# Optimization experiments

Hardware: AMD Instinct MI355X
Metric: run time of the kernel (lower is better)

The kernel has to match this reference:

```python
import jax, jax.numpy as jnp
import numpy as np

K_ORDER = 3
GRID_N = 10
GRID_LO, GRID_HI = -2.0, 2.0
LAYERS = [(49, 256), (256, 256), (256, 10)]
NCOEF = GRID_N + K_ORDER  # 13


def mish(x):
    return x * jnp.tanh(jax.nn.softplus(x))


def bspline_basis(x):
    # x: (B, in) -> basis (B, in, GRID_N + K_ORDER)
    h = (GRID_HI - GRID_LO) / GRID_N
    knots = GRID_LO + h * jnp.arange(-K_ORDER, GRID_N + K_ORDER + 1, dtype=x.dtype)  # (G+2k+1,)
    xx = x[..., None]
    B = ((xx >= knots[:-1]) & (xx < knots[1:])).astype(x.dtype)  # degree-0, (B,in,G+2k)
    for d in range(1, K_ORDER + 1):
        left = (xx - knots[: -(d + 1)]) / (knots[d:-1] - knots[: -(d + 1)]) * B[..., :-1]
        right = (knots[d + 1:] - xx) / (knots[d + 1:] - knots[1:-d]) * B[..., 1:]
        B = left + right
    return B  # (B, in, G+k)


def kan_layer(x, coef, scale_base, scale_sp, bias):
    # x: (B,in); coef: (in,out,G+k); scales: (in,out); bias: (out,)
    basis = bspline_basis(x)                                   # (B,in,G+k)
    spline = jnp.einsum('big,iog->bo', basis, coef * scale_sp[..., None])
    base = jnp.einsum('bi,io->bo', mish(x), scale_base)
    return base + spline + bias


def setup_inputs() -> dict:
    key = jax.random.key(0)
    ks = jax.random.split(key, 1 + 4 * len(LAYERS))
    inp = {'x': jax.random.normal(ks[0], (8192, 1, 28, 28), dtype=jnp.float32)}
    i = 1
    for li, (fin, fout) in enumerate(LAYERS, start=1):
        inp[f'coef{li}'] = 0.1 * jax.random.normal(ks[i], (fin, fout, NCOEF), dtype=jnp.float32); i += 1
        inp[f'sb{li}'] = 1.0 + 0.1 * jax.random.normal(ks[i], (fin, fout), dtype=jnp.float32); i += 1
        inp[f'sp{li}'] = 1.0 + 0.1 * jax.random.normal(ks[i], (fin, fout), dtype=jnp.float32); i += 1
        inp[f'b{li}'] = jnp.zeros((fout,), dtype=jnp.float32); i += 1
    return inp


def reference(x, coef1, sb1, sp1, b1, coef2, sb2, sp2, b2, coef3, sb3, sp3, b3):
    B = x.shape[0]
    # avg_pool2d(x, 4): 28x28 -> 7x7
    h = x.reshape(B, 1, 7, 4, 7, 4).mean(axis=(3, 5))
    h = h.reshape(B, 49)
    h = kan_layer(h, coef1, sb1, sp1, b1)
    h = kan_layer(h, coef2, sb2, sp2, b2)
    h = kan_layer(h, coef3, sb3, sp3, b3)
    return jax.nn.log_softmax(h, axis=1)
```

## Files before the change

### kernel.cpp

```cpp
#include <hip/hip_runtime.h>
#include <hip/hip_bf16.h>

typedef __bf16 bf16x8_t __attribute__((ext_vector_type(8)));
typedef float f32x4_t __attribute__((ext_vector_type(4)));
using bf16 = __hip_bfloat16;

#define ASG __attribute__((address_space(1)))
#define ASL __attribute__((address_space(3)))

__device__ __forceinline__ void gld_lds16(const void* g, void* l) {
  __builtin_amdgcn_global_load_lds((ASG void*)const_cast<void*>(g),
                                   (ASL void*)l, 16, 0, 0);
}

__device__ __forceinline__ unsigned short f2bf_bits(float v) {
  __hip_bfloat16 h = __float2bfloat16(v);
  return *reinterpret_cast<unsigned short*>(&h);
}

__device__ __forceinline__ float mish_f(float x) {
  float z = __expf(x);
  float n = z * (z + 2.0f);
  float m = x * n / (n + 2.0f);
  return (x > 10.0f) ? x : m;
}

__device__ __forceinline__ void kan_feats28(bf16* dst, float x) {
  unsigned int* d32 = (unsigned int*)dst;
#pragma unroll
  for (int d = 0; d < 7; ++d) d32[d] = 0u;
  float t = (x + 3.2f) * 2.5f;
  if (t >= 0.0f && t < 16.0f) {
    float tf = floorf(t);
    int c = (int)tf;
    float u = t - tf;
    float um = 1.0f - u;
    float u2 = u * u, u3 = u2 * u;
    const float s6 = 1.0f / 6.0f;
    float w0 = um * um * um * s6;
    float w1 = (3.0f * u3 - 6.0f * u2 + 4.0f) * s6;
    float w2 = (-3.0f * u3 + 3.0f * u2 + 3.0f * u + 1.0f) * s6;
    float w3 = u3 * s6;
    int j0 = c - 3;
    if (j0 >= 0)               dst[j0]     = __float2bfloat16(w0);
    if (j0 >= -1 && j0 <= 11)  dst[j0 + 1] = __float2bfloat16(w1);
    if (j0 >= -2 && j0 <= 10)  dst[j0 + 2] = __float2bfloat16(w2);
    if (j0 <= 9)               dst[j0 + 3] = __float2bfloat16(w3);
  }
  dst[13] = __float2bfloat16(mish_f(x));
}

__global__ __launch_bounds__(256) void prep_all(
    const float* __restrict__ c1, const float* __restrict__ sb1, const float* __restrict__ sp1,
    const float* __restrict__ c2, const float* __restrict__ sb2, const float* __restrict__ sp2,
    const float* __restrict__ c3, const float* __restrict__ sb3, const float* __restrict__ sp3,
    bf16* __restrict__ W1t, bf16* __restrict__ W2f, bf16* __restrict__ W3f) {
  const int b = blockIdx.x, o = threadIdx.x;
  float vals[14];
  if (b < 49) {
    const int i = b;
    const size_t io = (size_t)i * 256 + o;
    const float spv = sp1[io];
#pragma unroll
    for (int r = 0; r < 13; ++r) vals[r] = c1[io * 13 + r] * spv;
    vals[13] = sb1[io];
    unsigned int* dst = (unsigned int*)(W1t + (size_t)o * 704 + i * 14);
#pragma unroll
    for (int d = 0; d < 7; ++d)
      dst[d] = (unsigned int)f2bf_bits(vals[2 * d]) |
               ((unsigned int)f2bf_bits(vals[2 * d + 1]) << 16);
  } else if (b == 49) {
    unsigned int* dst = (unsigned int*)(W1t + (size_t)o * 704 + 686);
#pragma unroll
    for (int d = 0; d < 9; ++d) dst[d] = 0u;
  } else if (b < 306) {
    const int i = b - 50;
    const size_t io = (size_t)i * 256 + o;
    const float spv = sp2[io];
#pragma unroll
    for (int r = 0; r < 13; ++r) vals[r] = c2[io * 13 + r] * spv;
    vals[13] = sb2[io];
    const int ntg = o >> 4, lr = o & 15;
#pragma unroll
    for (int d = 0; d < 7; ++d) {
      const int k2 = i * 14 + 2 * d;
      const int kc = k2 / 224, rem = k2 % 224;
      const int ks = rem / 32, r2 = rem % 32, quad = r2 / 8, el = r2 % 8;
      const size_t off = ((size_t)((kc * 7 + ks) * 16 + ntg)) * 512 + lr * 32 + quad * 8 + el;
      *(unsigned int*)(W2f + off) = (unsigned int)f2bf_bits(vals[2 * d]) |
                                    ((unsigned int)f2bf_bits(vals[2 * d + 1]) << 16);
    }
  } else {
    const int i = b - 306;
    if (o < 10) {
      const size_t io = (size_t)i * 10 + o;
      const float spv = sp3[io];
#pragma unroll
      for (int r = 0; r < 13; ++r) vals[r] = c3[io * 13 + r] * spv;
      vals[13] = sb3[io];
#pragma unroll
      for (int d = 0; d < 7; ++d) {
        const int k2 = i * 14 + 2 * d;
        const int s = k2 >> 5, r2 = k2 & 31;
        const size_t off = (size_t)s * 512 + o * 32 + (r2 >> 3) * 8 + (r2 & 7);
        *(unsigned int*)(W3f + off) = (unsigned int)f2bf_bits(vals[2 * d]) |
                                      ((unsigned int)f2bf_bits(vals[2 * d + 1]) << 16);
      }
    } else if (o < 16) {
#pragma unroll
      for (int d = 0; d < 7; ++d) {
        const int k2 = i * 14 + 2 * d;
        const int s = k2 >> 5, r2 = k2 & 31;
        *(unsigned int*)(W3f + (size_t)s * 512 + o * 32 + (r2 >> 3) * 8 + (r2 & 7)) = 0u;
      }
    }
  }
}

__global__ __launch_bounds__(256) void pool_basis1(const float* __restrict__ x,
                                                   bf16* __restrict__ A1) {
  __shared__ __align__(16) float xs[3136];
  __shared__ __align__(16) bf16 arow[4 * 704];
  const int b4 = blockIdx.x * 4, t = threadIdx.x;
  const float4* xsrc = (const float4*)(x + (size_t)b4 * 784);
  float4* xd = (float4*)xs;
#pragma unroll
  for (int l = t; l < 784; l += 256) xd[l] = xsrc[l];
  __syncthreads();
  if (t < 196) {
    const int img = t / 49, p = t - img * 49;
    const int oh = p / 7, ow = p - oh * 7;
    const float* xi = xs + img * 784;
    float s = 0.f;
#pragma unroll
    for (int r = 0; r < 4; ++r)
#pragma unroll
      for (int c = 0; c < 4; ++c) s += xi[(oh * 4 + r) * 28 + ow * 4 + c];
    kan_feats28(&arow[img * 704 + p * 14], s * (1.0f / 16.0f));
  } else if (t < 232) {
    const int q = t - 196;
    const int img = q / 9, d = q - img * 9;
    ((unsigned int*)(arow + img * 704 + 686))[d] = 0u;
  }
  __syncthreads();
  uint4* dst = (uint4*)(A1 + (size_t)b4 * 704);
  const uint4* src = (const uint4*)arow;
#pragma unroll
  for (int l = t; l < 352; l += 256) dst[l] = src[l];
}

__global__ __launch_bounds__(256) void gemm1s(
    const bf16* __restrict__ A, const bf16* __restrict__ Wt,
    const float* __restrict__ bias, float* __restrict__ H) {
  constexpr int K = 704;
  __shared__ __align__(16) bf16 As[64 * 64];
  __shared__ __align__(16) bf16 Bs[64 * 64];
  const int t = threadIdx.x;
  const int wv = t >> 6, lane = t & 63, quad = lane >> 4, lr = lane & 15;
  const int n0 = blockIdx.x * 64;
  const int m0 = blockIdx.y * 64;
  const int srow0 = lane >> 3;
  const int cg = (lane & 7) ^ srow0;
  const bf16* gA0 = A + (size_t)(m0 + 8 * wv + srow0) * K + cg * 8;
  const bf16* gA1 = A + (size_t)(m0 + 32 + 8 * wv + srow0) * K + cg * 8;
  const bf16* gB0 = Wt + (size_t)(n0 + 8 * wv + srow0) * K + cg * 8;
  const bf16* gB1 = Wt + (size_t)(n0 + 32 + 8 * wv + srow0) * K + cg * 8;
  char* const lA = (char*)As + wv * 1024;
  char* const lB = (char*)Bs + wv * 1024;
  const int wm = (wv & 1) * 32, wn = (wv >> 1) * 32;
  const int swz = lr & 7;
  f32x4_t acc00 = {0.f, 0.f, 0.f, 0.f}, acc01 = acc00, acc10 = acc00, acc11 = acc00;
  for (int k0 = 0; k0 < K; k0 += 64) {
    gld_lds16(gA0 + k0, lA);
    gld_lds16(gA1 + k0, lA + 4096);
    gld_lds16(gB0 + k0, lB);
    gld_lds16(gB1 + k0, lB + 4096);
    __syncthreads();
#pragma unroll
    for (int s = 0; s < 2; ++s) {
      const int co = ((s * 4 + quad) ^ swz) * 16;
      bf16x8_t a0 = *(const bf16x8_t*)((char*)As + (wm + lr) * 128 + co);
      bf16x8_t a1 = *(const bf16x8_t*)((char*)As + (wm + 16 + lr) * 128 + co);
      bf16x8_t b0 = *(const bf16x8_t*)((char*)Bs + (wn + lr) * 128 + co);
      bf16x8_t b1 = *(const bf16x8_t*)((char*)Bs + (wn + 16 + lr) * 128 + co);
      acc00 = __builtin_amdgcn_mfma_f32_16x16x32_bf16(a0, b0, acc00, 0, 0, 0);
      acc01 = __builtin_amdgcn_mfma_f32_16x16x32_bf16(a0, b1, acc01, 0, 0, 0);
      acc10 = __builtin_amdgcn_mfma_f32_16x16x32_bf16(a1, b0, acc10, 0, 0, 0);
      acc11 = __builtin_amdgcn_mfma_f32_16x16x32_bf16(a1, b1, acc11, 0, 0, 0);
    }
    __syncthreads();
  }
  const int cb = n0 + wn + lr;
  const float bn0 = bias[cb], bn1 = bias[cb + 16];
#pragma unroll
  for (int r = 0; r < 4; ++r) {
    const size_t row = (size_t)(m0 + wm + quad * 4 + r);
    H[row * 256 + cb] = acc00[r] + bn0;
    H[row * 256 + cb + 16] = acc01[r] + bn1;
    H[(row + 16) * 256 + cb] = acc10[r] + bn0;
    H[(row + 16) * 256 + cb + 16] = acc11[r] + bn1;
  }
}

__global__ __launch_bounds__(512, 4) void kan_gemm2(
    const float* __restrict__ Hin, const bf16* __restrict__ W2f,
    float* __restrict__ Hp) {
  __shared__ __align__(16) bf16 As[2][64 * 232];
  const int t = threadIdx.x;
  const int w = t >> 6, lane = t & 63, quad = lane >> 4, lr = lane & 15;
  const int m0 = blockIdx.x * 64;
  const int z = blockIdx.y;
  const int ej = t & 15, er0 = (t >> 4) & 31;
  const int foff = lr * 32 + quad * 8;
  f32x4_t acc[4][2];
#pragma unroll
  for (int m = 0; m < 4; ++m) {
    acc[m][0] = (f32x4_t){0.f, 0.f, 0.f, 0.f};
    acc[m][1] = (f32x4_t){0.f, 0.f, 0.f, 0.f};
  }
  const float* hp = Hin + (size_t)(m0 + er0) * 256 + z * 64 + ej;
  kan_feats28(As[0] + er0 * 232 + ej * 14, hp[0]);
  kan_feats28(As[0] + (er0 + 32) * 232 + ej * 14, hp[32 * 256]);
  const bf16* wbase = W2f + ((size_t)(z * 28 * 16 + w * 2)) * 512 + foff;
  bf16x8_t p0[4], p1[4];
#pragma unroll
  for (int s = 0; s < 4; ++s) {
    p0[s] = *(const bf16x8_t*)(wbase + (size_t)s * 8192);
    p1[s] = *(const bf16x8_t*)(wbase + (size_t)s * 8192 + 512);
  }
#pragma unroll
  for (int kcl = 0; kcl < 4; ++kcl) {
    __syncthreads();
    const bf16* cur = As[kcl & 1];
    bf16* nxt = As[(kcl & 1) ^ 1];
#pragma unroll
    for (int ks = 0; ks < 7; ++ks) {
      const int step = kcl * 7 + ks;
      const int slot = step & 3;
      bf16x8_t b0 = p0[slot], b1 = p1[slot];
      if (step + 4 < 28) {
        p0[slot] = *(const bf16x8_t*)(wbase + (size_t)(step + 4) * 8192);
        p1[slot] = *(const bf16x8_t*)(wbase + (size_t)(step + 4) * 8192 + 512);
      }
#pragma unroll
      for (int m = 0; m < 4; ++m) {
        bf16x8_t a = *(const bf16x8_t*)(cur + (m * 16 + lr) * 232 + ks * 32 + quad * 8);
        acc[m][0] = __builtin_amdgcn_mfma_f32_16x16x32_bf16(a, b0, acc[m][0], 0, 0, 0);
        acc[m][1] = __builtin_amdgcn_mfma_f32_16x16x32_bf16(a, b1, acc[m][1], 0, 0, 0);
      }
    }
    if (kcl < 3) {
      kan_feats28(nxt + er0 * 232 + ej * 14, hp[(kcl + 1) * 16]);
      kan_feats28(nxt + (er0 + 32) * 232 + ej * 14, hp[32 * 256 + (kcl + 1) * 16]);
    }
  }
  float* Hpz = Hp + (size_t)z * (8192 * 256);
  const int c0 = w * 32 + lr;
#pragma unroll
  for (int m = 0; m < 4; ++m)
#pragma unroll
    for (int r = 0; r < 4; ++r) {
      const size_t row = (size_t)(m0 + m * 16 + quad * 4 + r);
      Hpz[row * 256 + c0] = acc[m][0][r];
      Hpz[row * 256 + c0 + 16] = acc[m][1][r];
    }
}

__global__ __launch_bounds__(256) void kan_gemm3(
    const float* __restrict__ Hp, const float* __restrict__ b2,
    const bf16* __restrict__ W3f, float* __restrict__ part) {
  __shared__ __align__(16) bf16 As[64 * 232];
  const int t = threadIdx.x;
  const int wv = t >> 6, lane = t & 63, quad = lane >> 4, lr = lane & 15;
  const int m0 = blockIdx.x * 64;
  const int z = blockIdx.y;
  const int ej = t & 15, er0 = t >> 4;
  const int foff = lr * 32 + quad * 8;
  f32x4_t acc = {0.f, 0.f, 0.f, 0.f};
#pragma unroll
  for (int kcl = 0; kcl < 2; ++kcl) {
    const int kc = z * 2 + kcl;
    const float bc = b2[kc * 16 + ej];
    const float* hp = Hp + (size_t)(m0 + er0) * 256 + kc * 16 + ej;
    if (kcl) __syncthreads();
#pragma unroll
    for (int e = 0; e < 4; ++e) {
      const size_t idx = (size_t)e * 16 * 256;
      float h = hp[idx] + hp[idx + 2097152] + hp[idx + 4194304] + hp[idx + 6291456] + bc;
      kan_feats28(As + (er0 + 16 * e) * 232 + ej * 14, h);
    }
    __syncthreads();
#pragma unroll
    for (int ks = 0; ks < 7; ++ks) {
      bf16x8_t b = *(const bf16x8_t*)(W3f + (size_t)(kc * 7 + ks) * 512 + foff);
      bf16x8_t a = *(const bf16x8_t*)(As + (wv * 16 + lr) * 232 + ks * 32 + quad * 8);
      acc = __builtin_amdgcn_mfma_f32_16x16x32_bf16(a, b, acc, 0, 0, 0);
    }
  }
#pragma unroll
  for (int r = 0; r < 4; ++r)
    part[(size_t)z * 131072 + (size_t)lr * 8192 + (m0 + wv * 16 + quad * 4 + r)] = acc[r];
}

__global__ __launch_bounds__(256) void lsm(const float* __restrict__ part,
                                           const float* __restrict__ b3,
                                           float* __restrict__ out) {
  const int row = blockIdx.x * 256 + threadIdx.x;
  float v[10];
#pragma unroll
  for (int o = 0; o < 10; ++o) {
    float s = b3[o];
#pragma unroll
    for (int kc = 0; kc < 8; ++kc) s += part[(size_t)kc * 131072 + (size_t)o * 8192 + row];
    v[o] = s;
  }
  float m = v[0];
#pragma unroll
  for (int o = 1; o < 10; ++o) m = fmaxf(m, v[o]);
  float se = 0.f;
#pragma unroll
  for (int o = 0; o < 10; ++o) se += expf(v[o] - m);
  const float l = m + logf(se);
#pragma unroll
  for (int o = 0; o < 10; ++o) out[(size_t)row * 10 + o] = v[o] - l;
}

extern "C" void kernel_launch(void* const* d_in, const int* in_sizes, int n_in,
                              void* d_out, int out_size, void* d_ws, size_t ws_size,
                              hipStream_t stream) {
  const float* x = (const float*)d_in[0];
  const float* coef1 = (const float*)d_in[1];
  const float* sb1 = (const float*)d_in[2];
  const float* sp1 = (const float*)d_in[3];
  const float* b1 = (const float*)d_in[4];
  const float* coef2 = (const float*)d_in[5];
  const float* sb2 = (const float*)d_in[6];
  const float* sp2 = (const float*)d_in[7];
  const float* b2 = (const float*)d_in[8];
  const float* coef3 = (const float*)d_in[9];
  const float* sb3 = (const float*)d_in[10];
  const float* sp3 = (const float*)d_in[11];
  const float* b3 = (const float*)d_in[12];
  float* out = (float*)d_out;

  char* ws = (char*)d_ws;
  size_t off = 0;
  bf16* A1 = (bf16*)(ws + off);    off += 11534336;
  bf16* W1t = (bf16*)(ws + off);   off += 360448;
  bf16* W2f = (bf16*)(ws + off);   off += 1835008;
  bf16* W3f = (bf16*)(ws + off);   off += 114688;
  float* H1 = (float*)(ws + off);  off += 8388608;
  float* Hp = (float*)(ws + off);  off += 33554432;
  float* part = (float*)(ws + off); off += 4194304;

  prep_all<<<562, 256, 0, stream>>>(coef1, sb1, sp1, coef2, sb2, sp2,
                                    coef3, sb3, sp3, W1t, W2f, W3f);
  pool_basis1<<<2048, 256, 0, stream>>>(x, A1);
  gemm1s<<<dim3(4, 128), 256, 0, stream>>>(A1, W1t, b1, H1);
  kan_gemm2<<<dim3(128, 4), 512, 0, stream>>>(H1, W2f, Hp);
  kan_gemm3<<<dim3(128, 8), 256, 0, stream>>>(Hp, b2, W3f, part);
  lsm<<<32, 256, 0, stream>>>(part, b3, out);
}
```

Measured before the change: 146.4 us.

## Fuse pooling, three KAN layers and log-softmax into one persistent kernel

Replaces the five-kernel chain (pool+basis, gemm1, gemm2, gemm3, log-softmax) with a single kernel in which each block processes 32 rows end to end. Intermediate activations stay in LDS instead of going through global workspace, and W1 is repacked into the same fragment layout as W2 so it can be streamed from registers. This removes several large global round trips and the launch gaps between kernels. The cost is a grid of only 256 blocks, each using about 120 KB of LDS and doing all the weight reads itself, so occupancy and weight reuse across rows drop.

```diff
diff --git a/kernel.cpp b/kernel.cpp
--- a/kernel.cpp
+++ b/kernel.cpp
@@ -4,14 +4,6 @@
 typedef __bf16 bf16x8_t __attribute__((ext_vector_type(8)));
 typedef float f32x4_t __attribute__((ext_vector_type(4)));
 using bf16 = __hip_bfloat16;
-
-#define ASG __attribute__((address_space(1)))
-#define ASL __attribute__((address_space(3)))
-
-__device__ __forceinline__ void gld_lds16(const void* g, void* l) {
-  __builtin_amdgcn_global_load_lds((ASG void*)const_cast<void*>(g),
-                                   (ASL void*)l, 16, 0, 0);
-}
 
 __device__ __forceinline__ unsigned short f2bf_bits(float v) {
   __hip_bfloat16 h = __float2bfloat16(v);
@@ -54,9 +46,10 @@
     const float* __restrict__ c1, const float* __restrict__ sb1, const float* __restrict__ sp1,
     const float* __restrict__ c2, const float* __restrict__ sb2, const float* __restrict__ sp2,
     const float* __restrict__ c3, const float* __restrict__ sb3, const float* __restrict__ sp3,
-    bf16* __restrict__ W1t, bf16* __restrict__ W2f, bf16* __restrict__ W3f) {
+    bf16* __restrict__ W1f, bf16* __restrict__ W2f, bf16* __restrict__ W3f) {
   const int b = blockIdx.x, o = threadIdx.x;
   float vals[14];
+  const int ntg = o >> 4, lrr = o & 15;
   if (b < 49) {
     const int i = b;
     const size_t io = (size_t)i * 256 + o;
@@ -64,15 +57,21 @@
 #pragma unroll
     for (int r = 0; r < 13; ++r) vals[r] = c1[io * 13 + r] * spv;
     vals[13] = sb1[io];
-    unsigned int* dst = (unsigned int*)(W1t + (size_t)o * 704 + i * 14);
-#pragma unroll
-    for (int d = 0; d < 7; ++d)
-      dst[d] = (unsigned int)f2bf_bits(vals[2 * d]) |
-               ((unsigned int)f2bf_bits(vals[2 * d + 1]) << 16);
+#pragma unroll
+    for (int d = 0; d < 7; ++d) {
+      const int k2 = i * 14 + 2 * d;
+      const int s = k2 >> 5, r2 = k2 & 31;
+      const size_t off = ((size_t)(s * 16 + ntg)) * 512 + lrr * 32 + (r2 >> 3) * 8 + (r2 & 7);
+      *(unsigned int*)(W1f + off) = (unsigned int)f2bf_bits(vals[2 * d]) |
+                                    ((unsigned int)f2bf_bits(vals[2 * d + 1]) << 16);
+    }
   } else if (b == 49) {
-    unsigned int* dst = (unsigned int*)(W1t + (size_t)o * 704 + 686);
-#pragma unroll
-    for (int d = 0; d < 9; ++d) dst[d] = 0u;
+#pragma unroll
+    for (int d = 0; d < 9; ++d) {
+      const int k2 = 686 + 2 * d;
+      const int r2 = k2 & 31;
+      *(unsigned int*)(W1f + ((size_t)(21 * 16 + ntg)) * 512 + lrr * 32 + (r2 >> 3) * 8 + (r2 & 7)) = 0u;
+    }
   } else if (b < 306) {
     const int i = b - 50;
     const size_t io = (size_t)i * 256 + o;
@@ -80,13 +79,11 @@
 #pragma unroll
     for (int r = 0; r < 13; ++r) vals[r] = c2[io * 13 + r] * spv;
     vals[13] = sb2[io];
-    const int ntg = o >> 4, lr = o & 15;
 #pragma unroll
     for (int d = 0; d < 7; ++d) {
       const int k2 = i * 14 + 2 * d;
-      const int kc = k2 / 224, rem = k2 % 224;
-      const int ks = rem / 32, r2 = rem % 32, quad = r2 / 8, el = r2 % 8;
-      const size_t off = ((size_t)((kc * 7 + ks) * 16 + ntg)) * 512 + lr * 32 + quad * 8 + el;
+      const int s = k2 >> 5, r2 = k2 & 31;
+      const size_t off = ((size_t)(s * 16 + ntg)) * 512 + lrr * 32 + (r2 >> 3) * 8 + (r2 & 7);
       *(unsigned int*)(W2f + off) = (unsigned int)f2bf_bits(vals[2 * d]) |
                                     ((unsigned int)f2bf_bits(vals[2 * d + 1]) << 16);
     }
@@ -117,212 +114,215 @@
   }
 }
 
-__global__ __launch_bounds__(256) void pool_basis1(const float* __restrict__ x,
-                                                   bf16* __restrict__ A1) {
-  __shared__ __align__(16) float xs[3136];
-  __shared__ __align__(16) bf16 arow[4 * 704];
-  const int b4 = blockIdx.x * 4, t = threadIdx.x;
-  const float4* xsrc = (const float4*)(x + (size_t)b4 * 784);
-  float4* xd = (float4*)xs;
-#pragma unroll
-  for (int l = t; l < 784; l += 256) xd[l] = xsrc[l];
-  __syncthreads();
-  if (t < 196) {
-    const int img = t / 49, p = t - img * 49;
-    const int oh = p / 7, ow = p - oh * 7;
-    const float* xi = xs + img * 784;
-    float s = 0.f;
-#pragma unroll
-    for (int r = 0; r < 4; ++r)
-#pragma unroll
-      for (int c = 0; c < 4; ++c) s += xi[(oh * 4 + r) * 28 + ow * 4 + c];
-    kan_feats28(&arow[img * 704 + p * 14], s * (1.0f / 16.0f));
-  } else if (t < 232) {
-    const int q = t - 196;
-    const int img = q / 9, d = q - img * 9;
-    ((unsigned int*)(arow + img * 704 + 686))[d] = 0u;
-  }
-  __syncthreads();
-  uint4* dst = (uint4*)(A1 + (size_t)b4 * 704);
-  const uint4* src = (const uint4*)arow;
-#pragma unroll
-  for (int l = t; l < 352; l += 256) dst[l] = src[l];
-}
-
-__global__ __launch_bounds__(256) void gemm1s(
-    const bf16* __restrict__ A, const bf16* __restrict__ Wt,
-    const float* __restrict__ bias, float* __restrict__ H) {
-  constexpr int K = 704;
-  __shared__ __align__(16) bf16 As[64 * 64];
-  __shared__ __align__(16) bf16 Bs[64 * 64];
-  const int t = threadIdx.x;
-  const int wv = t >> 6, lane = t & 63, quad = lane >> 4, lr = lane & 15;
-  const int n0 = blockIdx.x * 64;
-  const int m0 = blockIdx.y * 64;
-  const int srow0 = lane >> 3;
-  const int cg = (lane & 7) ^ srow0;
-  const bf16* gA0 = A + (size_t)(m0 + 8 * wv + srow0) * K + cg * 8;
-  const bf16* gA1 = A + (size_t)(m0 + 32 + 8 * wv + srow0) * K + cg * 8;
-  const bf16* gB0 = Wt + (size_t)(n0 + 8 * wv + srow0) * K + cg * 8;
-  const bf16* gB1 = Wt + (size_t)(n0 + 32 + 8 * wv + srow0) * K + cg * 8;
-  char* const lA = (char*)As + wv * 1024;
-  char* const lB = (char*)Bs + wv * 1024;
-  const int wm = (wv & 1) * 32, wn = (wv >> 1) * 32;
-  const int swz = lr & 7;
-  f32x4_t acc00 = {0.f, 0.f, 0.f, 0.f}, acc01 = acc00, acc10 = acc00, acc11 = acc00;
-  for (int k0 = 0; k0 < K; k0 += 64) {
-    gld_lds16(gA0 + k0, lA);
-    gld_lds16(gA1 + k0, lA + 4096);
-    gld_lds16(gB0 + k0, lB);
-    gld_lds16(gB1 + k0, lB + 4096);
-    __syncthreads();
-#pragma unroll
-    for (int s = 0; s < 2; ++s) {
-      const int co = ((s * 4 + quad) ^ swz) * 16;
-      bf16x8_t a0 = *(const bf16x8_t*)((char*)As + (wm + lr) * 128 + co);
-      bf16x8_t a1 = *(const bf16x8_t*)((char*)As + (wm + 16 + lr) * 128 + co);
-      bf16x8_t b0 = *(const bf16x8_t*)((char*)Bs + (wn + lr) * 128 + co);
-      bf16x8_t b1 = *(const bf16x8_t*)((char*)Bs + (wn + 16 + lr) * 128 + co);
-      acc00 = __builtin_amdgcn_mfma_f32_16x16x32_bf16(a0, b0, acc00, 0, 0, 0);
-      acc01 = __builtin_amdgcn_mfma_f32_16x16x32_bf16(a0, b1, acc01, 0, 0, 0);
-      acc10 = __builtin_amdgcn_mfma_f32_16x16x32_bf16(a1, b0, acc10, 0, 0, 0);
-      acc11 = __builtin_amdgcn_mfma_f32_16x16x32_bf16(a1, b1, acc11, 0, 0, 0);
-    }
-    __syncthreads();
-  }
-  const int cb = n0 + wn + lr;
-  const float bn0 = bias[cb], bn1 = bias[cb + 16];
-#pragma unroll
-  for (int r = 0; r < 4; ++r) {
-    const size_t row = (size_t)(m0 + wm + quad * 4 + r);
-    H[row * 256 + cb] = acc00[r] + bn0;
-    H[row * 256 + cb + 16] = acc01[r] + bn1;
-    H[(row + 16) * 256 + cb] = acc10[r] + bn0;
-    H[(row + 16) * 256 + cb + 16] = acc11[r] + bn1;
-  }
-}
-
-__global__ __launch_bounds__(512, 4) void kan_gemm2(
-    const float* __restrict__ Hin, const bf16* __restrict__ W2f,
-    float* __restrict__ Hp) {
-  __shared__ __align__(16) bf16 As[2][64 * 232];
+__global__ __launch_bounds__(512, 2) void meganet(
+    const float* __restrict__ x, const bf16* __restrict__ W1f,
+    const bf16* __restrict__ W2f, const bf16* __restrict__ W3f,
+    const float* __restrict__ b1, const float* __restrict__ b2,
+    const float* __restrict__ b3, float* __restrict__ out) {
+  __shared__ __align__(16) char lds[120320];
+  float* const xs = (float*)lds;
+  float* const P = (float*)(lds + 50176);
+  float* const Hs1 = (float*)lds;
+  bf16* const Ach0 = (bf16*)(lds + 57344);
+  bf16* const Ach1 = (bf16*)(lds + 72192);
+  float* const Hs2 = (float*)(lds + 87040);
+  float* const Red = (float*)lds;
+  float* const V = (float*)(lds + 14336);
+
   const int t = threadIdx.x;
   const int w = t >> 6, lane = t & 63, quad = lane >> 4, lr = lane & 15;
-  const int m0 = blockIdx.x * 64;
-  const int z = blockIdx.y;
-  const int ej = t & 15, er0 = (t >> 4) & 31;
+  const int tr = t >> 4, ej = t & 15;
+  const int r0 = blockIdx.x * 32;
+  const int ntg0 = w * 2;
   const int foff = lr * 32 + quad * 8;
-  f32x4_t acc[4][2];
-#pragma unroll
-  for (int m = 0; m < 4; ++m) {
-    acc[m][0] = (f32x4_t){0.f, 0.f, 0.f, 0.f};
-    acc[m][1] = (f32x4_t){0.f, 0.f, 0.f, 0.f};
-  }
-  const float* hp = Hin + (size_t)(m0 + er0) * 256 + z * 64 + ej;
-  kan_feats28(As[0] + er0 * 232 + ej * 14, hp[0]);
-  kan_feats28(As[0] + (er0 + 32) * 232 + ej * 14, hp[32 * 256]);
-  const bf16* wbase = W2f + ((size_t)(z * 28 * 16 + w * 2)) * 512 + foff;
-  bf16x8_t p0[4], p1[4];
+
+  for (int h = 0; h < 2; ++h) {
+    const float4* src = (const float4*)x + (size_t)(r0 + h * 16) * 196;
+    float4* xd = (float4*)xs;
+#pragma unroll
+    for (int l = 0; l < 7; ++l) {
+      const int idx = t + l * 512;
+      if (idx < 3136) xd[idx] = src[idx];
+    }
+    __syncthreads();
+    for (int task = t; task < 784; task += 512) {
+      const int img = task / 49, p = task - img * 49;
+      const int oh = p / 7, ow = p - oh * 7;
+      const float* xi = xs + img * 784 + oh * 112 + ow * 4;
+      float s = 0.f;
+#pragma unroll
+      for (int rr = 0; rr < 4; ++rr)
+#pragma unroll
+        for (int cc = 0; cc < 4; ++cc) s += xi[rr * 28 + cc];
+      P[(h * 16 + img) * 56 + p] = s * (1.0f / 16.0f);
+    }
+    __syncthreads();
+  }
+
+  f32x4_t acc1[2][2];
+#pragma unroll
+  for (int m = 0; m < 2; ++m)
+#pragma unroll
+    for (int n = 0; n < 2; ++n) acc1[m][n] = (f32x4_t){0.f, 0.f, 0.f, 0.f};
+  bf16x8_t qa[4], qb[4];
 #pragma unroll
   for (int s = 0; s < 4; ++s) {
-    p0[s] = *(const bf16x8_t*)(wbase + (size_t)s * 8192);
-    p1[s] = *(const bf16x8_t*)(wbase + (size_t)s * 8192 + 512);
-  }
-#pragma unroll
-  for (int kcl = 0; kcl < 4; ++kcl) {
-    __syncthreads();
-    const bf16* cur = As[kcl & 1];
-    bf16* nxt = As[(kcl & 1) ^ 1];
+    qa[s] = *(const bf16x8_t*)(W1f + (size_t)(s * 16 + ntg0) * 512 + foff);
+    qb[s] = *(const bf16x8_t*)(W1f + (size_t)(s * 16 + ntg0 + 1) * 512 + foff);
+  }
+  kan_feats28(Ach0 + tr * 232 + ej * 14, P[tr * 56 + ej]);
+  __syncthreads();
+#pragma unroll
+  for (int c = 0; c < 4; ++c) {
+    const bf16* const Ac = (c & 1) ? Ach1 : Ach0;
+    bf16* const An = (c & 1) ? Ach0 : Ach1;
+    const int nks = (c < 3) ? 7 : 1;
 #pragma unroll
     for (int ks = 0; ks < 7; ++ks) {
-      const int step = kcl * 7 + ks;
-      const int slot = step & 3;
-      bf16x8_t b0 = p0[slot], b1 = p1[slot];
-      if (step + 4 < 28) {
-        p0[slot] = *(const bf16x8_t*)(wbase + (size_t)(step + 4) * 8192);
-        p1[slot] = *(const bf16x8_t*)(wbase + (size_t)(step + 4) * 8192 + 512);
-      }
-#pragma unroll
-      for (int m = 0; m < 4; ++m) {
-        bf16x8_t a = *(const bf16x8_t*)(cur + (m * 16 + lr) * 232 + ks * 32 + quad * 8);
-        acc[m][0] = __builtin_amdgcn_mfma_f32_16x16x32_bf16(a, b0, acc[m][0], 0, 0, 0);
-        acc[m][1] = __builtin_amdgcn_mfma_f32_16x16x32_bf16(a, b1, acc[m][1], 0, 0, 0);
-      }
-    }
-    if (kcl < 3) {
-      kan_feats28(nxt + er0 * 232 + ej * 14, hp[(kcl + 1) * 16]);
-      kan_feats28(nxt + (er0 + 32) * 232 + ej * 14, hp[32 * 256 + (kcl + 1) * 16]);
-    }
-  }
-  float* Hpz = Hp + (size_t)z * (8192 * 256);
-  const int c0 = w * 32 + lr;
-#pragma unroll
-  for (int m = 0; m < 4; ++m)
-#pragma unroll
-    for (int r = 0; r < 4; ++r) {
-      const size_t row = (size_t)(m0 + m * 16 + quad * 4 + r);
-      Hpz[row * 256 + c0] = acc[m][0][r];
-      Hpz[row * 256 + c0 + 16] = acc[m][1][r];
-    }
-}
-
-__global__ __launch_bounds__(256) void kan_gemm3(
-    const float* __restrict__ Hp, const float* __restrict__ b2,
-    const bf16* __restrict__ W3f, float* __restrict__ part) {
-  __shared__ __align__(16) bf16 As[64 * 232];
-  const int t = threadIdx.x;
-  const int wv = t >> 6, lane = t & 63, quad = lane >> 4, lr = lane & 15;
-  const int m0 = blockIdx.x * 64;
-  const int z = blockIdx.y;
-  const int ej = t & 15, er0 = t >> 4;
-  const int foff = lr * 32 + quad * 8;
-  f32x4_t acc = {0.f, 0.f, 0.f, 0.f};
-#pragma unroll
-  for (int kcl = 0; kcl < 2; ++kcl) {
-    const int kc = z * 2 + kcl;
-    const float bc = b2[kc * 16 + ej];
-    const float* hp = Hp + (size_t)(m0 + er0) * 256 + kc * 16 + ej;
-    if (kcl) __syncthreads();
-#pragma unroll
-    for (int e = 0; e < 4; ++e) {
-      const size_t idx = (size_t)e * 16 * 256;
-      float h = hp[idx] + hp[idx + 2097152] + hp[idx + 4194304] + hp[idx + 6291456] + bc;
-      kan_feats28(As + (er0 + 16 * e) * 232 + ej * 14, h);
-    }
-    __syncthreads();
+      if (ks >= nks) continue;
+      const int kk = c * 7 + ks;
+      const int sl = kk & 3;
+      bf16x8_t bb0 = qa[sl], bb1 = qb[sl];
+      if (kk + 4 < 22) {
+        qa[sl] = *(const bf16x8_t*)(W1f + (size_t)((kk + 4) * 16 + ntg0) * 512 + foff);
+        qb[sl] = *(const bf16x8_t*)(W1f + (size_t)((kk + 4) * 16 + ntg0 + 1) * 512 + foff);
+      }
+#pragma unroll
+      for (int m = 0; m < 2; ++m) {
+        bf16x8_t a = *(const bf16x8_t*)(Ac + (m * 16 + lr) * 232 + ks * 32 + quad * 8);
+        acc1[m][0] = __builtin_amdgcn_mfma_f32_16x16x32_bf16(a, bb0, acc1[m][0], 0, 0, 0);
+        acc1[m][1] = __builtin_amdgcn_mfma_f32_16x16x32_bf16(a, bb1, acc1[m][1], 0, 0, 0);
+      }
+    }
+    if (c < 2) {
+      kan_feats28(An + tr * 232 + ej * 14, P[tr * 56 + (c + 1) * 16 + ej]);
+    } else if (c == 2) {
+      if (ej == 0) kan_feats28(An + tr * 232, P[tr * 56 + 48]);
+      else if (ej == 1) {
+        unsigned int* z = (unsigned int*)(An + tr * 232 + 14);
+#pragma unroll
+        for (int d = 0; d < 9; ++d) z[d] = 0u;
+      }
+    }
+    __syncthreads();
+  }
+#pragma unroll
+  for (int m = 0; m < 2; ++m)
+#pragma unroll
+    for (int n = 0; n < 2; ++n) {
+      const int col = w * 32 + n * 16 + lr;
+      const float bn = b1[col];
+#pragma unroll
+      for (int r = 0; r < 4; ++r)
+        Hs1[(m * 16 + quad * 4 + r) * 260 + col] = acc1[m][n][r] + bn;
+    }
+  __syncthreads();
+
+  f32x4_t acc2[2][2];
+#pragma unroll
+  for (int m = 0; m < 2; ++m)
+#pragma unroll
+    for (int n = 0; n < 2; ++n) acc2[m][n] = (f32x4_t){0.f, 0.f, 0.f, 0.f};
+#pragma unroll
+  for (int s = 0; s < 4; ++s) {
+    qa[s] = *(const bf16x8_t*)(W2f + (size_t)(s * 16 + ntg0) * 512 + foff);
+    qb[s] = *(const bf16x8_t*)(W2f + (size_t)(s * 16 + ntg0 + 1) * 512 + foff);
+  }
+  kan_feats28(Ach0 + tr * 232 + ej * 14, Hs1[tr * 260 + ej]);
+  __syncthreads();
+#pragma unroll
+  for (int c = 0; c < 16; ++c) {
+    const bf16* const Ac = (c & 1) ? Ach1 : Ach0;
+    bf16* const An = (c & 1) ? Ach0 : Ach1;
 #pragma unroll
     for (int ks = 0; ks < 7; ++ks) {
-      bf16x8_t b = *(const bf16x8_t*)(W3f + (size_t)(kc * 7 + ks) * 512 + foff);
-      bf16x8_t a = *(const bf16x8_t*)(As + (wv * 16 + lr) * 232 + ks * 32 + quad * 8);
-      acc = __builtin_amdgcn_mfma_f32_16x16x32_bf16(a, b, acc, 0, 0, 0);
-    }
-  }
-#pragma unroll
-  for (int r = 0; r < 4; ++r)
-    part[(size_t)z * 131072 + (size_t)lr * 8192 + (m0 + wv * 16 + quad * 4 + r)] = acc[r];
-}
-
-__global__ __launch_bounds__(256) void lsm(const float* __restrict__ part,
-                                           const float* __restrict__ b3,
-                                           float* __restrict__ out) {
-  const int row = blockIdx.x * 256 + threadIdx.x;
-  float v[10];
-#pragma unroll
-  for (int o = 0; o < 10; ++o) {
-    float s = b3[o];
-#pragma unroll
-    for (int kc = 0; kc < 8; ++kc) s += part[(size_t)kc * 131072 + (size_t)o * 8192 + row];
-    v[o] = s;
-  }
-  float m = v[0];
-#pragma unroll
-  for (int o = 1; o < 10; ++o) m = fmaxf(m, v[o]);
-  float se = 0.f;
-#pragma unroll
-  for (int o = 0; o < 10; ++o) se += expf(v[o] - m);
-  const float l = m + logf(se);
-#pragma unroll
-  for (int o = 0; o < 10; ++o) out[(size_t)row * 10 + o] = v[o] - l;
+      const int kk = c * 7 + ks;
+      const int sl = kk & 3;
+      bf16x8_t bb0 = qa[sl], bb1 = qb[sl];
+      if (kk + 4 < 112) {
+        qa[sl] = *(const bf16x8_t*)(W2f + (size_t)((kk + 4) * 16 + ntg0) * 512 + foff);
+        qb[sl] = *(const bf16x8_t*)(W2f + (size_t)((kk + 4) * 16 + ntg0 + 1) * 512 + foff);
+      }
+#pragma unroll
+      for (int m = 0; m < 2; ++m) {
+        bf16x8_t a = *(const bf16x8_t*)(Ac + (m * 16 + lr) * 232 + ks * 32 + quad * 8);
+        acc2[m][0] = __builtin_amdgcn_mfma_f32_16x16x32_bf16(a, bb0, acc2[m][0], 0, 0, 0);
+        acc2[m][1] = __builtin_amdgcn_mfma_f32_16x16x32_bf16(a, bb1, acc2[m][1], 0, 0, 0);
+      }
+    }
+    if (c < 15)
+      kan_feats28(An + tr * 232 + ej * 14, Hs1[tr * 260 + (c + 1) * 16 + ej]);
+    __syncthreads();
+  }
+#pragma unroll
+  for (int m = 0; m < 2; ++m)
+#pragma unroll
+    for (int n = 0; n < 2; ++n) {
+      const int col = w * 32 + n * 16 + lr;
+      const float bn = b2[col];
+#pragma unroll
+      for (int r = 0; r < 4; ++r)
+        Hs2[(m * 16 + quad * 4 + r) * 260 + col] = acc2[m][n][r] + bn;
+    }
+  __syncthreads();
+
+  f32x4_t acc3[2];
+  acc3[0] = (f32x4_t){0.f, 0.f, 0.f, 0.f};
+  acc3[1] = acc3[0];
+  bf16x8_t w3q[2];
+  if (w < 7) {
+    w3q[0] = *(const bf16x8_t*)(W3f + (size_t)(0 * 7 + w) * 512 + foff);
+    w3q[1] = *(const bf16x8_t*)(W3f + (size_t)(1 * 7 + w) * 512 + foff);
+  }
+  kan_feats28(Ach0 + tr * 232 + ej * 14, Hs2[tr * 260 + ej]);
+  __syncthreads();
+#pragma unroll
+  for (int c = 0; c < 16; ++c) {
+    const bf16* const Ac = (c & 1) ? Ach1 : Ach0;
+    bf16* const An = (c & 1) ? Ach0 : Ach1;
+    if (w < 7) {
+      bf16x8_t bb = w3q[c & 1];
+      if (c + 2 < 16)
+        w3q[c & 1] = *(const bf16x8_t*)(W3f + (size_t)((c + 2) * 7 + w) * 512 + foff);
+#pragma unroll
+      for (int m = 0; m < 2; ++m) {
+        bf16x8_t a = *(const bf16x8_t*)(Ac + (m * 16 + lr) * 232 + w * 32 + quad * 8);
+        acc3[m] = __builtin_amdgcn_mfma_f32_16x16x32_bf16(a, bb, acc3[m], 0, 0, 0);
+      }
+    }
+    if (c < 15)
+      kan_feats28(An + tr * 232 + ej * 14, Hs2[tr * 260 + (c + 1) * 16 + ej]);
+    __syncthreads();
+  }
+  if (w < 7) {
+#pragma unroll
+    for (int m = 0; m < 2; ++m)
+#pragma unroll
+      for (int r = 0; r < 4; ++r)
+        Red[w * 512 + (m * 16 + quad * 4 + r) * 16 + lr] = acc3[m][r];
+  }
+  __syncthreads();
+  {
+    float s = (ej < 10) ? b3[ej] : 0.f;
+#pragma unroll
+    for (int wv = 0; wv < 7; ++wv) s += Red[wv * 512 + tr * 16 + ej];
+    V[tr * 16 + ej] = s;
+  }
+  __syncthreads();
+  if (t < 32) {
+    float vv[10];
+#pragma unroll
+    for (int o = 0; o < 10; ++o) vv[o] = V[t * 16 + o];
+    float mx = vv[0];
+#pragma unroll
+    for (int o = 1; o < 10; ++o) mx = fmaxf(mx, vv[o]);
+    float se = 0.f;
+#pragma unroll
+    for (int o = 0; o < 10; ++o) se += expf(vv[o] - mx);
+    const float l = mx + logf(se);
+#pragma unroll
+    for (int o = 0; o < 10; ++o) out[(size_t)(r0 + t) * 10 + o] = vv[o] - l;
+  }
 }
 
 extern "C" void kernel_launch(void* const* d_in, const int* in_sizes, int n_in,
@@ -344,20 +344,11 @@
   float* out = (float*)d_out;
 
   char* ws = (char*)d_ws;
-  size_t off = 0;
-  bf16* A1 = (bf16*)(ws + off);    off += 11534336;
-  bf16* W1t = (bf16*)(ws + off);   off += 360448;
-  bf16* W2f = (bf16*)(ws + off);   off += 1835008;
-  bf16* W3f = (bf16*)(ws + off);   off += 114688;
-  float* H1 = (float*)(ws + off);  off += 8388608;
-  float* Hp = (float*)(ws + off);  off += 33554432;
-  float* part = (float*)(ws + off); off += 4194304;
+  bf16* W1f = (bf16*)ws;
+  bf16* W2f = (bf16*)(ws + 360448);
+  bf16* W3f = (bf16*)(ws + 2195456);
 
   prep_all<<<562, 256, 0, stream>>>(coef1, sb1, sp1, coef2, sb2, sp2,
-                                    coef3, sb3, sp3, W1t, W2f, W3f);
-  pool_basis1<<<2048, 256, 0, stream>>>(x, A1);
-  gemm1s<<<dim3(4, 128), 256, 0, stream>>>(A1, W1t, b1, H1);
-  kan_gemm2<<<dim3(128, 4), 512, 0, stream>>>(H1, W2f, Hp);
-  kan_gemm3<<<dim3(128, 8), 256, 0, stream>>>(Hp, b2, W3f, part);
-  lsm<<<32, 256, 0, stream>>>(part, b3, out);
-}
+                                    coef3, sb3, sp3, W1f, W2f, W3f);
+  meganet<<<256, 512, 0, stream>>>(x, W1f, W2f, W3f, b1, b2, b3, out);
+}
```

After: 141.1 us. 1.04x faster.
